# Kernel tuning notes

Hardware: AMD Instinct MI355X
Metric: run time of the kernel (lower is better)

Reference implementation:

```python
import jax, jax.numpy as jnp
import numpy as np

B, S, DIM, HEADS, HEAD_DIM = 4, 1024, 1024, 16, 64
INNER = HEADS * HEAD_DIM
NEG_INF = -1e30


def _rotate_half(t):
    # interleaved pairs: (x1, x2) -> (-x2, x1)
    t = t.reshape(*t.shape[:-1], -1, 2)
    x1, x2 = t[..., 0], t[..., 1]
    return jnp.stack((-x2, x1), axis=-1).reshape(*t.shape[:-2], -1)


def _apply_rope(t, freqs, scale):
    # t: [B, S, INNER]; freqs: [1, S, rot_dim]; rotate only first rot_dim channels
    rot_dim = freqs.shape[-1]
    t_rot, t_pass = t[..., :rot_dim], t[..., rot_dim:]
    t_rot = t_rot * jnp.cos(freqs) * scale + _rotate_half(t_rot) * jnp.sin(freqs) * scale
    return jnp.concatenate((t_rot, t_pass), axis=-1)


def setup_inputs() -> dict:
    key = jax.random.key(0)
    ks = jax.random.split(key, 12)
    x = jax.random.normal(ks[0], (B, S, DIM), dtype=jnp.float32)
    mask = jax.random.bernoulli(ks[1], 0.9, (B, S))
    mask = mask.at[:, 0].set(True)  # ensure every row has a valid key
    # standard rope angles, interleave-repeated to head_dim
    pos = np.arange(S, dtype=np.float32)
    inv_freq = 1.0 / (10000.0 ** (np.arange(0, HEAD_DIM, 2, dtype=np.float32) / HEAD_DIM))
    ang = pos[:, None] * inv_freq[None, :]             # [S, HEAD_DIM//2]
    freqs = jnp.asarray(np.repeat(ang, 2, axis=-1)[None])  # [1, S, HEAD_DIM]
    sc = 1.0 / np.sqrt(DIM)
    def lin(k, din, dout):
        kw, kb = jax.random.split(k)
        return (jax.random.uniform(kw, (din, dout), minval=-sc, maxval=sc),
                jax.random.uniform(kb, (dout,), minval=-sc, maxval=sc))
    Wq, bq = lin(ks[2], DIM, INNER)
    Wk, bk = lin(ks[3], DIM, INNER)
    Wv, bv = lin(ks[4], DIM, INNER)
    Wo, bo = lin(ks[5], INNER, DIM)
    return {"x": x, "mask": mask, "freqs": freqs, "Wq": Wq, "bq": bq,
            "Wk": Wk, "bk": bk, "Wv": Wv, "bv": bv, "Wo": Wo, "bo": bo}


def reference(x, mask, freqs, Wq, bq, Wk, bk, Wv, bv, Wo, bo):
    b = x.shape[0]
    q = x @ Wq + bq
    k = x @ Wk + bk
    v = x @ Wv + bv
    # xpos_scale is None -> scale 1.0 for both q and k
    q = _apply_rope(q, freqs, 1.0)
    k = _apply_rope(k, freqs, 1.0)
    # split heads: [B, H, S, Dh]
    q = q.reshape(b, -1, HEADS, HEAD_DIM).transpose(0, 2, 1, 3)
    k = k.reshape(b, -1, HEADS, HEAD_DIM).transpose(0, 2, 1, 3)
    v = v.reshape(b, -1, HEADS, HEAD_DIM).transpose(0, 2, 1, 3)
    scores = jnp.einsum('bhqd,bhkd->bhqk', q, k) / jnp.sqrt(jnp.float32(HEAD_DIM))
    scores = jnp.where(mask[:, None, None, :], scores, NEG_INF)
    attn = jax.nn.softmax(scores, axis=-1)
    out = jnp.einsum('bhqk,bhkd->bhqd', attn, v)
    out = out.transpose(0, 2, 1, 3).reshape(b, -1, INNER)
    out = out @ Wo + bo
    out = jnp.where(mask[..., None], out, 0.0)
    return out
```

## Files before the change

kernel.cpp:

```cpp
#include <hip/hip_runtime.h>
#include <stdint.h>


typedef unsigned short u16;
typedef __attribute__((ext_vector_type(8))) short short8;
typedef __attribute__((ext_vector_type(4))) float f32x4;
typedef __attribute__((ext_vector_type(4))) unsigned short bf4;

#define LOG2E 1.44269504088896f
#define INV2PI 0.15915494309189535f
#define MFMA_BF16(a,b,c) __builtin_amdgcn_mfma_f32_16x16x32_bf16((a),(b),(c),0,0,0)

__device__ __forceinline__ float bf2f(u16 u){
    union { uint32_t i; float f; } v; v.i = ((uint32_t)u) << 16; return v.f;
}
__device__ __forceinline__ u16 f2bf(float f){
    uint32_t u = __builtin_bit_cast(uint32_t, f);
    u += 0x7FFFu + ((u >> 16) & 1u);
    return (u16)(u >> 16);
}
__device__ __forceinline__ uint32_t cvt_pk_bf16(float lo, float hi){
    uint32_t r;
    asm("v_cvt_pk_bf16_f32 %0, %1, %2" : "=v"(r) : "v"(lo), "v"(hi));
    return r;
}
__device__ __forceinline__ float fast_ex2(float x){
    float r; asm("v_exp_f32 %0, %1" : "=v"(r) : "v"(x)); return r;
}
__device__ __forceinline__ float fast_rcp(float x){
    float r; asm("v_rcp_f32 %0, %1" : "=v"(r) : "v"(x)); return r;
}
__device__ __forceinline__ void fast_sincos(float xrad, float& s, float& c){
    float rev = xrad * INV2PI, fr;
    asm("v_fract_f32 %0, %1" : "=v"(fr) : "v"(rev));
    asm("v_cos_f32 %0, %1" : "=v"(c) : "v"(fr));
    asm("v_sin_f32 %0, %1" : "=v"(s) : "v"(fr));
}

__device__ __forceinline__ void gload_lds16(const void* g, uint32_t dst_lds_byte){
    __builtin_amdgcn_global_load_lds(
        (__attribute__((address_space(1))) uint32_t*)(uintptr_t)g,
        (__attribute__((address_space(3))) uint32_t*)(uintptr_t)dst_lds_byte,
        16, 0, 0);
}

constexpr size_t OFF_XB    = 0;
constexpr size_t OFF_VT    = OFF_XB;
constexpr size_t OFF_WQKVT = 8388608;
constexpr size_t OFF_WOT   = OFF_WQKVT + 6291456;
constexpr size_t OFF_BQKV  = OFF_WOT   + 2097152;
constexpr size_t OFF_MASKB = OFF_BQKV  + 12288;
constexpr size_t OFF_QKV   = OFF_MASKB + 16384;
constexpr size_t OFF_AO    = OFF_QKV   + 25165824;
constexpr size_t WS_NEED   = OFF_AO    + 8388608;

__global__ __launch_bounds__(256) void k_prep(const float* __restrict__ x,
                                              const float* __restrict__ Wq,
                                              const float* __restrict__ Wk,
                                              const float* __restrict__ Wv,
                                              const float* __restrict__ Wo,
                                              const float* __restrict__ bq,
                                              const float* __restrict__ bk,
                                              const float* __restrict__ bv,
                                              const unsigned char* __restrict__ mask,
                                              u16* __restrict__ xb,
                                              u16* __restrict__ Wqkvt,
                                              u16* __restrict__ Wot,
                                              float* __restrict__ bqkv,
                                              float* __restrict__ maskb){
    __shared__ float lds[64][65];
    const int t = threadIdx.x, bid = blockIdx.x;
    if (bid < 4096){
        int gid = bid * 256 + t;
        float4 v = ((const float4*)x)[gid];
        bf4 o;
        o[0] = f2bf(v.x); o[1] = f2bf(v.y); o[2] = f2bf(v.z); o[3] = f2bf(v.w);
        ((bf4*)xb)[gid] = o;
    } else if (bid < 5120){
        int blk = bid - 4096;
        int which = blk >> 8;
        const float* src = which == 0 ? Wq : which == 1 ? Wk : which == 2 ? Wv : Wo;
        u16* dst = which < 3 ? (Wqkvt + (size_t)which * 1024 * 1024) : Wot;
        int n0 = ((blk >> 4) & 15) * 64, k0 = (blk & 15) * 64;
        #pragma unroll
        for (int i = 0; i < 16; i++){
            int idx = t + i * 256; int rr = idx >> 6, cc = idx & 63;
            lds[rr][cc] = src[(size_t)(k0 + rr) * 1024 + n0 + cc];
        }
        __syncthreads();
        #pragma unroll
        for (int i = 0; i < 16; i++){
            int idx = t + i * 256; int rr = idx >> 6, cc = idx & 63;
            dst[(size_t)(n0 + rr) * 1024 + k0 + cc] = f2bf(lds[cc][rr]);
        }
    } else {
        int gid = (bid - 5120) * 256 + t;
        if (gid < 3072){
            bqkv[gid] = gid < 1024 ? bq[gid] : gid < 2048 ? bk[gid - 1024] : bv[gid - 2048];
        } else if (gid < 3072 + 4096){
            int j = gid - 3072;
            int cnt3f = 0;
            #pragma unroll
            for (int i = 0; i < 16; i++) cnt3f += (mask[4 * i + 3] == 0x3F);
            bool v;
            if (cnt3f >= 8){
                v = ((const float*)mask)[j] != 0.f;
            } else {
                int nz = 0;
                for (int i = 1; i < 64; i++) if (i & 3) nz += (mask[i] != 0);
                if (nz) v = mask[j] != 0;
                else    v = ((const int*)mask)[j] != 0;
            }
            maskb[j] = v ? 0.f : -1e30f;
        }
    }
}

template<bool QKV>
__global__ __launch_bounds__(256) void k_gemm(const u16* __restrict__ A,
                                              const u16* __restrict__ Bt,
                                              const float* __restrict__ bias,
                                              const float* __restrict__ maskb,
                                              const float* __restrict__ freqs,
                                              void* __restrict__ Cout,
                                              int M, int N, int K){
    __shared__ alignas(16) u16 sA[128 * 32];
    __shared__ alignas(16) u16 sB[128 * 32];
    const int t = threadIdx.x;
    const int w = t >> 6, l = t & 63, g = l >> 4, r = l & 15;
    const int brow = blockIdx.x * 128, bcol = blockIdx.y * 128;
    const int wr = (w >> 1) * 64, wc = (w & 1) * 64;
    f32x4 acc[4][4] = {};

    const int lrow = w * 32 + (l >> 2);
    const int lcol = (l & 3) * 8;
    const u16* ga = A  + (size_t)(brow + lrow) * K + lcol;
    const u16* gb = Bt + (size_t)(bcol + lrow) * K + lcol;
    const size_t K16 = (size_t)16 * K;
    uint32_t dstA = (uint32_t)__builtin_amdgcn_readfirstlane(
        (int)((uint32_t)(uintptr_t)&sA[0] + (uint32_t)(w * 2048)));
    uint32_t dstB = (uint32_t)__builtin_amdgcn_readfirstlane(
        (int)((uint32_t)(uintptr_t)&sB[0] + (uint32_t)(w * 2048)));

    for (int k0 = 0; k0 < K; k0 += 32){
        gload_lds16(ga + k0,       dstA);
        gload_lds16(ga + k0 + K16, dstA + 1024);
        gload_lds16(gb + k0,       dstB);
        gload_lds16(gb + k0 + K16, dstB + 1024);
        __syncthreads();
        short8 af[4], bf[4];
        #pragma unroll
        for (int m = 0; m < 4; m++) af[m] = *(const short8*)&sA[(wr + m * 16 + r) * 32 + g * 8];
        #pragma unroll
        for (int n = 0; n < 4; n++) bf[n] = *(const short8*)&sB[(wc + n * 16 + r) * 32 + g * 8];
        __builtin_amdgcn_s_setprio(1);
        #pragma unroll
        for (int m = 0; m < 4; m++)
            #pragma unroll
            for (int n = 0; n < 4; n++)
                acc[m][n] = MFMA_BF16(af[m], bf[n], acc[m][n]);
        __builtin_amdgcn_s_setprio(0);
        __syncthreads();
    }

    const bool rope = QKV && (bcol == 0 || bcol == 1024) && (wc == 0);
    #pragma unroll
    for (int n = 0; n < 4; n++){
        int col = bcol + wc + n * 16 + r;
        float bb = bias[col];
        float cs = (QKV && col < 1024) ? 0.125f : 1.f;
        #pragma unroll
        for (int m = 0; m < 4; m++){
            f32x4 v = acc[m][n];
            #pragma unroll
            for (int jj = 0; jj < 4; jj++){
                int row = brow + wr + m * 16 + g * 4 + jj;
                float val = (v[jj] + bb) * cs;
                if (QKV){
                    if (rope){
                        float partner = __shfl_xor(val, 1);
                        float ang = freqs[(row & 1023) * 64 + (col & 62)];
                        float sn, c;
                        fast_sincos(ang, sn, c);
                        val = (r & 1) ? val * c + partner * sn
                                      : val * c - partner * sn;
                    }
                    ((u16*)Cout)[(size_t)row * N + col] = f2bf(val);
                } else {
                    ((float*)Cout)[(size_t)row * N + col] =
                        (maskb[row] == 0.f) ? val : 0.f;
                }
            }
        }
    }
}

__global__ __launch_bounds__(256) void k_vt(const u16* __restrict__ QKV,
                                            u16* __restrict__ Vt){
    __shared__ u16 lds[64][72];
    const int bh = blockIdx.x >> 4, s0 = (blockIdx.x & 15) * 64;
    const int b = bh >> 4, h = bh & 15;
    const int t = threadIdx.x;
    const u16* src = QKV + (size_t)(b * 1024 + s0) * 3072 + 2048 + h * 64;
    #pragma unroll
    for (int i = 0; i < 2; i++){
        int s = i * 32 + (t >> 3), dc = (t & 7) * 8;
        short8 v = *(const short8*)(src + (size_t)s * 3072 + dc);
        #pragma unroll
        for (int j = 0; j < 8; j++) lds[dc + j][s] = (u16)v[j];
    }
    __syncthreads();
    #pragma unroll
    for (int i = 0; i < 2; i++){
        int d = i * 32 + (t >> 3), sc = (t & 7) * 8;
        short8 v = *(const short8*)&lds[d][sc];
        *(short8*)&Vt[(size_t)(bh * 64 + d) * 1024 + s0 + sc] = v;
    }
}

__global__ __launch_bounds__(256) void k_attn(const u16* __restrict__ QKV,
                                              const u16* __restrict__ Vt,
                                              const float* __restrict__ maskb,
                                              u16* __restrict__ AO){
    __shared__ alignas(16) u16 sK [2][64 * 64];
    __shared__ alignas(16) u16 sVt[2][64 * 64];
    __shared__ alignas(16) u16 sP [4][16 * 64];
    const int t = threadIdx.x, w = t >> 6, l = t & 63, g = l >> 4, r = l & 15;
    const int hw = blockIdx.x;
    const int blk = ((hw & 7) << 7) | (hw >> 3);
    const int qb = blk & 15, h = (blk >> 4) & 15, b = blk >> 8;
    const int bh = b * 16 + h;
    const int qrow0 = b * 1024 + qb * 64 + w * 16;
    const int rx = r & 7;

    const u16* qptr = QKV + (size_t)(qrow0 + r) * 3072 + h * 64;
    short8 qf0 = *(const short8*)(qptr + g * 8);
    short8 qf1 = *(const short8*)(qptr + 32 + g * 8);

    const int srow = l >> 3;
    const int c16  = (l & 7) ^ srow;
    const u16* Kg = QKV + (size_t)(b * 1024) * 3072 + 1024 + h * 64;
    const u16* gK0 = Kg + (size_t)(w * 16 + srow) * 3072 + c16 * 8;
    const u16* gK1 = gK0 + (size_t)8 * 3072;
    const u16* Vg = Vt + (size_t)bh * 64 * 1024;
    const u16* gV0 = Vg + (size_t)(w * 16 + srow) * 1024 + c16 * 8;
    const u16* gV1 = gV0 + (size_t)8 * 1024;
    uint32_t dK0 = (uint32_t)__builtin_amdgcn_readfirstlane(
        (int)((uint32_t)(uintptr_t)&sK[0][0] + (uint32_t)(w * 2048)));
    uint32_t dV0 = (uint32_t)__builtin_amdgcn_readfirstlane(
        (int)((uint32_t)(uintptr_t)&sVt[0][0] + (uint32_t)(w * 2048)));
    char* sPw = (char*)&sP[w][0];
    const char* sKc = (const char*)&sK[0][0];
    const char* sVc = (const char*)&sVt[0][0];

    const float* mkb = maskb + b * 1024;

    f32x4 oacc[4] = {};
    float lsum = 0.f;

    gload_lds16(gK0, dK0);
    gload_lds16(gK1, dK0 + 1024);
    gload_lds16(gV0, dV0);
    gload_lds16(gV1, dV0 + 1024);
    __syncthreads();

    for (int kt = 0; kt < 16; ++kt){
        const int cur = kt & 1;
        if (kt < 15){
            const size_t kv = (size_t)(kt + 1) * 64;
            const uint32_t dk = dK0 + (cur ^ 1) * 8192;
            const uint32_t dv = dV0 + (cur ^ 1) * 8192;
            gload_lds16(gK0 + kv * 3072, dk);
            gload_lds16(gK1 + kv * 3072, dk + 1024);
            gload_lds16(gV0 + kv, dv);
            gload_lds16(gV1 + kv, dv + 1024);
        }
        const char* sKb = sKc + cur * 8192;
        const char* sVb = sVc + cur * 8192;
        const int kv0 = kt * 64;

        f32x4 st[4];
        __builtin_amdgcn_s_setprio(1);
        #pragma unroll
        for (int kn = 0; kn < 4; kn++){
            const int row = kn * 16 + r;
            short8 kf0 = *(const short8*)(sKb + row * 128 + (((g    ) ^ rx) << 4));
            short8 kf1 = *(const short8*)(sKb + row * 128 + (((g + 4) ^ rx) << 4));
            f32x4 z = {};
            z = MFMA_BF16(kf0, qf0, z);
            st[kn] = MFMA_BF16(kf1, qf1, z);
        }
        __builtin_amdgcn_s_setprio(0);

        float p[16];
        #pragma unroll
        for (int kn = 0; kn < 4; kn++){
            f32x4 mbv = *(const f32x4*)(mkb + kv0 + kn * 16 + g * 4);
            #pragma unroll
            for (int jj = 0; jj < 4; jj++){
                float pe = fast_ex2(fmaf(st[kn][jj], LOG2E, mbv[jj]));
                p[kn * 4 + jj] = pe;
                lsum += pe;
            }
        }

        #pragma unroll
        for (int kn = 0; kn < 4; kn++){
            uint2 u;
            u.x = cvt_pk_bf16(p[kn * 4 + 0], p[kn * 4 + 1]);
            u.y = cvt_pk_bf16(p[kn * 4 + 2], p[kn * 4 + 3]);
            *(uint2*)(sPw + r * 128 + ((((2 * kn + (g >> 1))) ^ rx) << 4) + (g & 1) * 8) = u;
        }

        #pragma unroll
        for (int ks = 0; ks < 2; ks++){
            short8 pa = *(const short8*)(sPw + r * 128 + ((((ks << 2) | g) ^ rx) << 4));
            __builtin_amdgcn_s_setprio(1);
            #pragma unroll
            for (int dn = 0; dn < 4; dn++){
                const int vrow = dn * 16 + r;
                short8 vf = *(const short8*)(sVb + vrow * 128 + ((((ks << 2) | g) ^ rx) << 4));
                oacc[dn] = MFMA_BF16(pa, vf, oacc[dn]);
            }
            __builtin_amdgcn_s_setprio(0);
        }
        __syncthreads();
    }

    lsum += __shfl_xor(lsum, 16);
    lsum += __shfl_xor(lsum, 32);
    float linv = fast_rcp(lsum);
    float lf[4];
    #pragma unroll
    for (int jj = 0; jj < 4; jj++) lf[jj] = __shfl(linv, g * 4 + jj);
    #pragma unroll
    for (int dn = 0; dn < 4; dn++)
        #pragma unroll
        for (int jj = 0; jj < 4; jj++)
            AO[(size_t)(qrow0 + g * 4 + jj) * 1024 + h * 64 + dn * 16 + r]
                = f2bf(oacc[dn][jj] * lf[jj]);
}

extern "C" void kernel_launch(void* const* d_in, const int* in_sizes, int n_in,
                              void* d_out, int out_size, void* d_ws, size_t ws_size,
                              hipStream_t stream){
    (void)in_sizes; (void)n_in; (void)out_size;
    if (ws_size < WS_NEED) return;

    const float* x     = (const float*)d_in[0];
    const unsigned char* mask = (const unsigned char*)d_in[1];
    const float* freqs = (const float*)d_in[2];
    const float* Wq    = (const float*)d_in[3];
    const float* bq    = (const float*)d_in[4];
    const float* Wk    = (const float*)d_in[5];
    const float* bk    = (const float*)d_in[6];
    const float* Wv    = (const float*)d_in[7];
    const float* bv    = (const float*)d_in[8];
    const float* Wo    = (const float*)d_in[9];
    const float* bo    = (const float*)d_in[10];

    char* ws = (char*)d_ws;
    u16*   xb    = (u16*)  (ws + OFF_XB);
    u16*   Vtw   = (u16*)  (ws + OFF_VT);
    u16*   Wqkvt = (u16*)  (ws + OFF_WQKVT);
    u16*   Wot   = (u16*)  (ws + OFF_WOT);
    float* bqkv  = (float*)(ws + OFF_BQKV);
    float* maskb = (float*)(ws + OFF_MASKB);
    u16*   QKV   = (u16*)  (ws + OFF_QKV);
    u16*   AO    = (u16*)  (ws + OFF_AO);

    k_prep<<<5148, 256, 0, stream>>>(x, Wq, Wk, Wv, Wo, bq, bk, bv, mask,
                                     xb, Wqkvt, Wot, bqkv, maskb);
    k_gemm<true><<<dim3(32, 24), 256, 0, stream>>>(xb, Wqkvt, bqkv, nullptr,
                                                   freqs, QKV, 4096, 3072, 1024);
    k_vt  <<<1024, 256, 0, stream>>>(QKV, Vtw);
    k_attn<<<1024, 256, 0, stream>>>(QKV, Vtw, maskb, AO);
    k_gemm<false><<<dim3(32, 8), 256, 0, stream>>>(AO, Wot, bo, maskb,
                                                   nullptr, d_out, 4096, 1024, 1024);
}
```

Baseline: 128.6 us.

## Pipeline GEMM K-loop with 4-stage LDS ring and prefetch depth two

Replaces the single-buffer load-sync-compute-sync loop in the GEMM kernel with a 4-slot LDS ring buffer, issuing global-to-LDS loads two K-tiles ahead. It uses explicit vmcnt waits plus a single barrier per iteration instead of two __syncthreads. The goal is to overlap global memory latency with MFMA work and cut barrier overhead. In exchange, LDS use per block grows to 64KB, which can limit occupancy, and correctness depends on the ring depth covering the missing trailing barrier.

Result: faster. 108.4 us (-15.7%).

```diff
diff --git a/kernel.cpp b/kernel.cpp
--- a/kernel.cpp
+++ b/kernel.cpp
@@ -10,6 +10,7 @@
 #define LOG2E 1.44269504088896f
 #define INV2PI 0.15915494309189535f
 #define MFMA_BF16(a,b,c) __builtin_amdgcn_mfma_f32_16x16x32_bf16((a),(b),(c),0,0,0)
+#define WAITV(N) asm volatile("s_waitcnt vmcnt(" #N ")" ::: "memory")
 
 __device__ __forceinline__ float bf2f(u16 u){
     union { uint32_t i; float f; } v; v.i = ((uint32_t)u) << 16; return v.f;
@@ -124,8 +125,7 @@
                                               const float* __restrict__ freqs,
                                               void* __restrict__ Cout,
                                               int M, int N, int K){
-    __shared__ alignas(16) u16 sA[128 * 32];
-    __shared__ alignas(16) u16 sB[128 * 32];
+    __shared__ alignas(16) u16 sAB[4][2][128 * 32];
     const int t = threadIdx.x;
     const int w = t >> 6, l = t & 63, g = l >> 4, r = l & 15;
     const int brow = blockIdx.x * 128, bcol = blockIdx.y * 128;
@@ -137,17 +137,30 @@
     const u16* ga = A  + (size_t)(brow + lrow) * K + lcol;
     const u16* gb = Bt + (size_t)(bcol + lrow) * K + lcol;
     const size_t K16 = (size_t)16 * K;
-    uint32_t dstA = (uint32_t)__builtin_amdgcn_readfirstlane(
-        (int)((uint32_t)(uintptr_t)&sA[0] + (uint32_t)(w * 2048)));
-    uint32_t dstB = (uint32_t)__builtin_amdgcn_readfirstlane(
-        (int)((uint32_t)(uintptr_t)&sB[0] + (uint32_t)(w * 2048)));
-
-    for (int k0 = 0; k0 < K; k0 += 32){
-        gload_lds16(ga + k0,       dstA);
-        gload_lds16(ga + k0 + K16, dstA + 1024);
-        gload_lds16(gb + k0,       dstB);
-        gload_lds16(gb + k0 + K16, dstB + 1024);
-        __syncthreads();
+    const uint32_t dst0 = (uint32_t)__builtin_amdgcn_readfirstlane(
+        (int)((uint32_t)(uintptr_t)&sAB[0][0][0] + (uint32_t)(w * 2048)));
+
+    const int NT = K >> 5;
+    auto stage = [&](int kt, int s){
+        const int k0 = kt * 32;
+        const uint32_t da = dst0 + (uint32_t)s * 16384;
+        gload_lds16(ga + k0,       da);
+        gload_lds16(ga + k0 + K16, da + 1024);
+        gload_lds16(gb + k0,       da + 8192);
+        gload_lds16(gb + k0 + K16, da + 8192 + 1024);
+    };
+
+    stage(0, 0);
+    stage(1, 1);
+    for (int kt = 0; kt < NT; ++kt){
+        if (kt + 2 < NT) stage(kt + 2, (kt + 2) & 3);
+        if      (kt + 2 < NT) WAITV(8);
+        else if (kt + 1 < NT) WAITV(4);
+        else                  WAITV(0);
+        __builtin_amdgcn_s_barrier();
+        __builtin_amdgcn_sched_barrier(0);
+        const u16* sA = &sAB[kt & 3][0][0];
+        const u16* sB = &sAB[kt & 3][1][0];
         short8 af[4], bf[4];
         #pragma unroll
         for (int m = 0; m < 4; m++) af[m] = *(const short8*)&sA[(wr + m * 16 + r) * 32 + g * 8];
@@ -160,7 +173,6 @@
             for (int n = 0; n < 4; n++)
                 acc[m][n] = MFMA_BF16(af[m], bf[n], acc[m][n]);
         __builtin_amdgcn_s_setprio(0);
-        __syncthreads();
     }
 
     const bool rope = QKV && (bcol == 0 || bcol == 1024) && (wc == 0);
```
